# Performance work log

Hardware: AMD Instinct MI355X
Metric: run time of the kernel (lower is better)

The kernel has to match this reference:

```python
import jax, jax.numpy as jnp
import numpy as np

D_MODEL = 1024
N_HEADS = 16
HEAD_DIM = D_MODEL // N_HEADS
LN_EPS = 1e-5


def _linear_init(key, fan_in, fan_out):
    # xavier_uniform for weight, zeros for bias; torch Linear weight is [out, in]
    limit = float(np.sqrt(6.0 / (fan_in + fan_out)))
    w = jax.random.uniform(key, (fan_out, fan_in), jnp.float32, -limit, limit)
    b = jnp.zeros((fan_out,), jnp.float32)
    return w, b


def setup_inputs() -> dict:
    key = jax.random.key(0)
    ks = jax.random.split(key, 8)
    B, S, D = 4, 1024, D_MODEL
    query = jax.random.normal(ks[0], (B, S, D), jnp.float32)
    key_t = jax.random.normal(ks[1], (B, S, D), jnp.float32)
    value = jax.random.normal(ks[2], (B, S, D), jnp.float32)
    Wq, bq = _linear_init(ks[3], D, D)
    Wk, bk = _linear_init(ks[4], D, D)
    Wv, bv = _linear_init(ks[5], D, D)
    Wfq, bfq = _linear_init(ks[6], D, D)
    Wfk, bfk = _linear_init(ks[7], D, D)
    gamma_q = jnp.ones((D,), jnp.float32); beta_q = jnp.zeros((D,), jnp.float32)
    gamma_k = jnp.ones((D,), jnp.float32); beta_k = jnp.zeros((D,), jnp.float32)
    return {"query": query, "key": key_t, "value": value,
            "Wq": Wq, "bq": bq, "Wk": Wk, "bk": bk, "Wv": Wv, "bv": bv,
            "Wfq": Wfq, "bfq": bfq, "Wfk": Wfk, "bfk": bfk,
            "gamma_q": gamma_q, "beta_q": beta_q,
            "gamma_k": gamma_k, "beta_k": beta_k}


def _layernorm(x, gamma, beta):
    mu = jnp.mean(x, axis=-1, keepdims=True)
    var = jnp.mean(jnp.square(x - mu), axis=-1, keepdims=True)
    return (x - mu) * jax.lax.rsqrt(var + LN_EPS) * gamma + beta


def reference(query, key, value, Wq, bq, Wk, bk, Wv, bv, Wfq, bfq, Wfk, bfk,
              gamma_q, beta_q, gamma_k, beta_k):
    B, Sq, D = query.shape
    H, Hd = N_HEADS, HEAD_DIM
    scale = jnp.sqrt(jnp.asarray(Hd, jnp.float32))

    residual_q, residual_k = query, key
    # torch Linear: x @ W.T + b
    q = (query @ Wq.T + bq).reshape(B, Sq, H, Hd).transpose(0, 2, 1, 3)  # [B,H,Sq,Hd]
    k = (key @ Wk.T + bk).reshape(B, -1, H, Hd).transpose(0, 2, 1, 3)    # [B,H,Sk,Hd]
    v = (value @ Wv.T + bv).reshape(B, -1, H, Hd).transpose(0, 2, 1, 3)  # [B,H,Sv,Hd]

    # Q->K attention (dropout disabled / eval mode)
    energy = jnp.einsum('bhqd,bhkd->bhqk', q, k) / scale
    attn_q2k = jax.nn.softmax(energy, axis=-1)
    x_q = jnp.einsum('bhqk,bhkd->bhqd', attn_q2k, v)
    x_q = x_q.transpose(0, 2, 1, 3).reshape(B, Sq, D)

    # K->Q attention (shares V)
    energy_k = jnp.einsum('bhkd,bhqd->bhkq', k, q) / scale
    attn_k2q = jax.nn.softmax(energy_k, axis=-1)
    x_k = jnp.einsum('bhkq,bhqd->bhkd', attn_k2q, v)
    x_k = x_k.transpose(0, 2, 1, 3).reshape(B, -1, D)

    q_out = x_q @ Wfq.T + bfq
    query_out = _layernorm(residual_q + q_out, gamma_q, beta_q)
    k_out = x_k @ Wfk.T + bfk
    key_out = _layernorm(residual_k + k_out, gamma_k, beta_k)
    return (query_out, key_out)
```

## Files before the change

### kernel.cpp

```cpp
#include <hip/hip_runtime.h>

typedef unsigned short u16;
typedef unsigned int u32;
typedef __attribute__((ext_vector_type(8))) short short8;
typedef __attribute__((ext_vector_type(4))) float floatx4;
typedef __attribute__((ext_vector_type(16))) float f32x16;
typedef __attribute__((ext_vector_type(4))) u32 u32x4;

#define AS_GLOBAL __attribute__((address_space(1)))
#define AS_LDS    __attribute__((address_space(3)))

__device__ __forceinline__ float b2f(u16 v) {
  union { u32 u; float f; } x; x.u = ((u32)v) << 16; return x.f;
}
__device__ __forceinline__ u16 f2bf(float f) {
  union { float f; u32 u; } x; x.f = f;
  u32 r = (x.u + 0x7fffu + ((x.u >> 16) & 1u)) >> 16;
  return (u16)r;
}
__device__ __forceinline__ u32 pk2(float lo, float hi) {
  u32 r; asm("v_cvt_pk_bf16_f32 %0, %1, %2" : "=v"(r) : "v"(lo), "v"(hi)); return r;
}
__device__ __forceinline__ float exp2_hw(float x) {
  float r; asm("v_exp_f32 %0, %1" : "=v"(r) : "v"(x)); return r;
}
__device__ __forceinline__ void plswap(u32& a, u32& b) {
  __attribute__((ext_vector_type(2))) unsigned int r =
      __builtin_amdgcn_permlane32_swap(a, b, false, false);
  a = r[0]; b = r[1];
}
__device__ __forceinline__ void gl_lds16(const u16* g, u16* l) {
  __builtin_amdgcn_global_load_lds((const AS_GLOBAL u32*)g, (AS_LDS u32*)l, 16, 0, 0);
}

__global__ __launch_bounds__(256)
void cvt8(const float* __restrict__ s0, const float* __restrict__ s1, const float* __restrict__ s2,
          const float* __restrict__ s3, const float* __restrict__ s4, const float* __restrict__ s5,
          const float* __restrict__ s6, const float* __restrict__ s7,
          u16* __restrict__ d0, u16* __restrict__ d1, u16* __restrict__ d2,
          u16* __restrict__ d3, u16* __restrict__ d4, u16* __restrict__ d5,
          u16* __restrict__ d6, u16* __restrict__ d7, int nbig, int nsmall)
{
  const int z = blockIdx.y;
  const float* s; u16* d; int n;
  switch (z) {
    case 0: s = s0; d = d0; n = nbig; break;
    case 1: s = s1; d = d1; n = nbig; break;
    case 2: s = s2; d = d2; n = nbig; break;
    case 3: s = s3; d = d3; n = nsmall; break;
    case 4: s = s4; d = d4; n = nsmall; break;
    case 5: s = s5; d = d5; n = nsmall; break;
    case 6: s = s6; d = d6; n = nsmall; break;
    default: s = s7; d = d7; n = nsmall; break;
  }
  const size_t idx = ((size_t)blockIdx.x * 256 + threadIdx.x) * 8;
  if (idx >= (size_t)n) return;
  float4 a0 = *(const float4*)(s + idx);
  float4 a1 = *(const float4*)(s + idx + 4);
  u16 t[8];
  t[0] = f2bf(a0.x); t[1] = f2bf(a0.y); t[2] = f2bf(a0.z); t[3] = f2bf(a0.w);
  t[4] = f2bf(a1.x); t[5] = f2bf(a1.y); t[6] = f2bf(a1.z); t[7] = f2bf(a1.w);
  *(uint4*)(d + idx) = *(const uint4*)t;
}

template <int TRANS2>
__global__ __launch_bounds__(256, 3)
void gemm_nt_bias(const u16* __restrict__ A0, const u16* __restrict__ W0, const float* __restrict__ B0, u16* __restrict__ C0,
                  const u16* __restrict__ A1, const u16* __restrict__ W1, const float* __restrict__ B1, u16* __restrict__ C1,
                  const u16* __restrict__ A2, const u16* __restrict__ W2, const float* __restrict__ B2, u16* __restrict__ C2)
{
  constexpr int K = 1024, N = 1024;
  __shared__ __attribute__((aligned(16))) u16 As[128 * 64];
  __shared__ __attribute__((aligned(16))) u16 Bs[128 * 64];

  const int z = blockIdx.z;
  const u16*   A  = z == 0 ? A0 : (z == 1 ? A1 : A2);
  const u16*   W  = z == 0 ? W0 : (z == 1 ? W1 : W2);
  const float* Bi = z == 0 ? B0 : (z == 1 ? B1 : B2);
  u16*         C  = z == 0 ? C0 : (z == 1 ? C1 : C2);

  const int tid  = threadIdx.x;
  const int lane = tid & 63;
  const int wave = tid >> 6;
  const int l32  = lane & 31;
  const int hi   = lane >> 5;
  const int wm = wave >> 1, wn = wave & 1;
  const int m0 = blockIdx.x * 128;
  const int n0 = blockIdx.y * 128;

  f32x16 acc[2][2];
#pragma unroll
  for (int i = 0; i < 2; ++i)
#pragma unroll
    for (int j = 0; j < 2; ++j)
#pragma unroll
      for (int e = 0; e < 16; ++e) acc[i][j][e] = 0.f;

  const int rr = lane >> 3;
  const int s7 = lane & 7;
  int scg[4];
#pragma unroll
  for (int i = 0; i < 4; ++i)
    scg[i] = ((s7 ^ rr ^ ((wave * 32 + i * 8) >> 3)) & 7) << 3;

  const u16* gA = A + (size_t)(m0 + wave * 32 + rr) * K;
  const u16* gW = W + (size_t)(n0 + wave * 32 + rr) * K;

  int offA0[4], offA1[4], offW0[4], offW1[4];
  {
    const int rA0 = wm * 64 + l32,      rA1 = rA0 + 32;
    const int rW0 = wn * 64 + l32,      rW1 = rW0 + 32;
    const int kA0 = (rA0 ^ (rA0 >> 3)) & 7, kA1 = (rA1 ^ (rA1 >> 3)) & 7;
    const int kW0 = (rW0 ^ (rW0 >> 3)) & 7, kW1 = (rW1 ^ (rW1 >> 3)) & 7;
#pragma unroll
    for (int ks = 0; ks < 4; ++ks) {
      const int g = ks * 2 + hi;
      offA0[ks] = rA0 * 64 + ((g ^ kA0) & 7) * 8;
      offA1[ks] = rA1 * 64 + ((g ^ kA1) & 7) * 8;
      offW0[ks] = rW0 * 64 + ((g ^ kW0) & 7) * 8;
      offW1[ks] = rW1 * 64 + ((g ^ kW1) & 7) * 8;
    }
  }

  const bool tr = TRANS2 && (z == 2);

  for (int k0 = 0; k0 < K; k0 += 64) {
#pragma unroll
    for (int i = 0; i < 4; ++i) {
      gl_lds16(gA + (size_t)(i * 8) * K + k0 + scg[i], &As[(wave * 32 + i * 8) * 64]);
      gl_lds16(gW + (size_t)(i * 8) * K + k0 + scg[i], &Bs[(wave * 32 + i * 8) * 64]);
    }
    __syncthreads();
    if (!tr) {
#pragma unroll
      for (int ks = 0; ks < 4; ++ks) {
        short8 fA0 = *(const short8*)&As[offA0[ks]];
        short8 fA1 = *(const short8*)&As[offA1[ks]];
        short8 fW0 = *(const short8*)&Bs[offW0[ks]];
        short8 fW1 = *(const short8*)&Bs[offW1[ks]];
        acc[0][0] = __builtin_amdgcn_mfma_f32_32x32x16_bf16(fW0, fA0, acc[0][0], 0, 0, 0);
        acc[0][1] = __builtin_amdgcn_mfma_f32_32x32x16_bf16(fW1, fA0, acc[0][1], 0, 0, 0);
        acc[1][0] = __builtin_amdgcn_mfma_f32_32x32x16_bf16(fW0, fA1, acc[1][0], 0, 0, 0);
        acc[1][1] = __builtin_amdgcn_mfma_f32_32x32x16_bf16(fW1, fA1, acc[1][1], 0, 0, 0);
      }
    } else {
#pragma unroll
      for (int ks = 0; ks < 4; ++ks) {
        short8 fA0 = *(const short8*)&As[offA0[ks]];
        short8 fA1 = *(const short8*)&As[offA1[ks]];
        short8 fW0 = *(const short8*)&Bs[offW0[ks]];
        short8 fW1 = *(const short8*)&Bs[offW1[ks]];
        acc[0][0] = __builtin_amdgcn_mfma_f32_32x32x16_bf16(fA0, fW0, acc[0][0], 0, 0, 0);
        acc[0][1] = __builtin_amdgcn_mfma_f32_32x32x16_bf16(fA0, fW1, acc[0][1], 0, 0, 0);
        acc[1][0] = __builtin_amdgcn_mfma_f32_32x32x16_bf16(fA1, fW0, acc[1][0], 0, 0, 0);
        acc[1][1] = __builtin_amdgcn_mfma_f32_32x32x16_bf16(fA1, fW1, acc[1][1], 0, 0, 0);
      }
    }
    __syncthreads();
  }

  if (!tr) {
    float4 bb[2][4];
#pragma unroll
    for (int nh = 0; nh < 2; ++nh)
#pragma unroll
      for (int q2 = 0; q2 < 4; ++q2)
        bb[nh][q2] = *(const float4*)&Bi[n0 + wn * 64 + nh * 32 + q2 * 8 + hi * 4];
#pragma unroll
    for (int mh = 0; mh < 2; ++mh) {
      u16* crow = C + (size_t)(m0 + wm * 64 + mh * 32 + l32) * N + n0 + wn * 64;
#pragma unroll
      for (int nh = 0; nh < 2; ++nh)
#pragma unroll
        for (int q2 = 0; q2 < 4; ++q2) {
          uint2 w;
          w.x = pk2(acc[mh][nh][q2 * 4 + 0] + bb[nh][q2].x,
                    acc[mh][nh][q2 * 4 + 1] + bb[nh][q2].y);
          w.y = pk2(acc[mh][nh][q2 * 4 + 2] + bb[nh][q2].z,
                    acc[mh][nh][q2 * 4 + 3] + bb[nh][q2].w);
          *(uint2*)(crow + nh * 32 + q2 * 8 + hi * 4) = w;
        }
    }
  } else {
    const float b0 = Bi[n0 + wn * 64 + l32];
    const float b1 = Bi[n0 + wn * 64 + 32 + l32];
#pragma unroll
    for (int nh = 0; nh < 2; ++nh) {
      const float bbv = nh ? b1 : b0;
      u16* ct = C + (size_t)(n0 + wn * 64 + nh * 32 + l32) * 4096 + m0 + wm * 64;
#pragma unroll
      for (int mh = 0; mh < 2; ++mh)
#pragma unroll
        for (int q2 = 0; q2 < 4; ++q2) {
          uint2 w;
          w.x = pk2(acc[mh][nh][q2 * 4 + 0] + bbv, acc[mh][nh][q2 * 4 + 1] + bbv);
          w.y = pk2(acc[mh][nh][q2 * 4 + 2] + bbv, acc[mh][nh][q2 * 4 + 3] + bbv);
          *(uint2*)(ct + mh * 32 + q2 * 8 + hi * 4) = w;
        }
    }
  }
}

__global__ __launch_bounds__(256, 2)
void flash32(const u16* __restrict__ Qg, const u16* __restrict__ Kg,
             const u16* __restrict__ VTw, u16* __restrict__ OQ, u16* __restrict__ OK)
{
  __shared__ __attribute__((aligned(16))) u16 smem[4 * 4096];

  const int tid = threadIdx.x;
  const int lane = tid & 63;
  const int wave = tid >> 6;
  const int l32 = lane & 31;
  const int hi = lane >> 5;

  const int jlin = blockIdx.x + 4 * (blockIdx.y + 64 * blockIdx.z);
  const int L = (jlin & 7) * 64 + (jlin >> 3);
  const int qx = L & 3;
  const int by = (L >> 2) & 63;
  const int bz = L >> 8;
  const int b = by >> 4, h = by & 15;
  const int q0 = qx * 256;

  const u16* Qw = bz ? Kg : Qg;
  const u16* Kw = bz ? Qg : Kg;
  u16* Ow = bz ? OK : OQ;

  const int rr = lane >> 3;
  const int s7 = lane & 7;

  const u16* Qt = Qw + ((size_t)(b * 1024 + q0)) * 1024 + h * 64;
  const u16* Kt = Kw + ((size_t)(b * 1024)) * 1024 + h * 64;
  const u16* Vt = VTw + ((size_t)(h * 64)) * 4096 + (size_t)b * 1024;

#pragma unroll
  for (int c = 0; c < 8; ++c) {
    const int R = wave * 64 + c * 8;
    const int cg = ((s7 ^ rr ^ (R >> 3)) & 7) << 3;
    gl_lds16(Qt + (size_t)(R + rr) * 1024 + cg, smem + R * 64);
  }
  __syncthreads();

  short8 aqA[4], aqB[4];
  {
    const int qrA = wave * 64 + l32, qrB = qrA + 32;
    const int kA = (qrA ^ (qrA >> 3)) & 7, kB = (qrB ^ (qrB >> 3)) & 7;
    const u16* bA = smem + qrA * 64;
    const u16* bB = smem + qrB * 64;
#pragma unroll
    for (int d2 = 0; d2 < 4; ++d2) {
      const int g = d2 * 2 + hi;
      aqA[d2] = *(const short8*)(bA + ((g ^ kA) & 7) * 8);
      aqB[d2] = *(const short8*)(bB + ((g ^ kB) & 7) * 8);
    }
  }
  __syncthreads();

  const int R0 = wave * 16, R1 = wave * 16 + 8;
  const int cg0 = ((s7 ^ rr ^ (R0 >> 3)) & 7) << 3;
  const int cg1 = ((s7 ^ rr ^ (R1 >> 3)) & 7) << 3;
  {
    u16* kd = smem + wave * 1024;
    u16* vd = smem + 8192 + wave * 1024;
    gl_lds16(Kt + (size_t)(R0 + rr) * 1024 + cg0, kd);
    gl_lds16(Kt + (size_t)(R1 + rr) * 1024 + cg1, kd + 512);
    gl_lds16(Vt + (size_t)(R0 + rr) * 4096 + cg0, vd);
    gl_lds16(Vt + (size_t)(R1 + rr) * 4096 + cg1, vd + 512);
  }
  __syncthreads();

  const int key0 = (l32 ^ (l32 >> 3)) & 7;
  const int key1 = key0 ^ 4;

  int offA[4], offB[4];
#pragma unroll
  for (int j = 0; j < 4; ++j) {
    const int g = j * 2 + hi;
    offA[j] = (l32 * 64 + ((g ^ key0) & 7) * 8) * 2;
    offB[j] = ((32 + l32) * 64 + ((g ^ key1) & 7) * 8) * 2;
  }

  const u16* pK0 = Kt + (size_t)(64 + R0 + rr) * 1024 + cg0;
  const u16* pK1 = Kt + (size_t)(64 + R1 + rr) * 1024 + cg1;
  const u16* pV0 = Vt + (size_t)(R0 + rr) * 4096 + 64 + cg0;
  const u16* pV1 = Vt + (size_t)(R1 + rr) * 4096 + 64 + cg1;

  f32x16 accO0A, accO1A, accO0B, accO1B;
#pragma unroll
  for (int i = 0; i < 16; ++i) {
    accO0A[i] = 0.f; accO1A[i] = 0.f; accO0B[i] = 0.f; accO1B[i] = 0.f;
  }
  f32x16 zeroS;
#pragma unroll
  for (int i = 0; i < 16; ++i) zeroS[i] = 0.f;

  float lsumA = 0.f, lsumB = 0.f;
  const float SCL2 = 0.18033688011112042f;
  const float MFIX2 = 10.098865286222744f;

#define EXP4(SV, o)                                                     \
  SV[o + 0] = exp2_hw(fmaf(SV[o + 0], SCL2, -MFIX2));                   \
  SV[o + 1] = exp2_hw(fmaf(SV[o + 1], SCL2, -MFIX2));                   \
  SV[o + 2] = exp2_hw(fmaf(SV[o + 2], SCL2, -MFIX2));                   \
  SV[o + 3] = exp2_hw(fmaf(SV[o + 3], SCL2, -MFIX2));
#define SUM8(v, o) (((v[o] + v[o + 1]) + (v[o + 2] + v[o + 3])) + \
                    ((v[o + 4] + v[o + 5]) + (v[o + 6] + v[o + 7])))
#define PACK(SV, PFA, PFB)                                              \
  {                                                                     \
    u32 a0 = pk2(SV[0], SV[1]),   a1 = pk2(SV[2], SV[3]);               \
    u32 b0 = pk2(SV[4], SV[5]),   b1 = pk2(SV[6], SV[7]);               \
    u32 c0 = pk2(SV[8], SV[9]),   c1 = pk2(SV[10], SV[11]);             \
    u32 d0 = pk2(SV[12], SV[13]), d1 = pk2(SV[14], SV[15]);             \
    plswap(a0, b0); plswap(a1, b1); plswap(c0, d0); plswap(c1, d1);     \
    u32x4 u0; u0[0] = a0; u0[1] = a1; u0[2] = b0; u0[3] = b1;           \
    u32x4 u1; u1[0] = c0; u1[1] = c1; u1[2] = d0; u1[3] = d1;           \
    PFA = __builtin_bit_cast(short8, u0);                               \
    PFB = __builtin_bit_cast(short8, u1);                               \
  }

  for (int jt = 0; jt < 16; ++jt) {
    const int cur = jt & 1;
    const char* ksb = (const char*)smem + cur * 8192;
    const char* vtb = (const char*)smem + 16384 + cur * 8192;

    if (jt < 15) {
      u16* kd = smem + (cur ^ 1) * 4096 + wave * 1024;
      u16* vd = smem + 8192 + (cur ^ 1) * 4096 + wave * 1024;
      gl_lds16(pK0, kd);
      gl_lds16(pK1, kd + 512);
      gl_lds16(pV0, vd);
      gl_lds16(pV1, vd + 512);
      pK0 += 65536; pK1 += 65536; pV0 += 64; pV1 += 64;
    }

    f32x16 sA0, sB0, sA1, sB1;
    {
      short8 kf = *(const short8*)(ksb + offA[0]);
      sA0 = __builtin_amdgcn_mfma_f32_32x32x16_bf16(kf, aqA[0], zeroS, 0, 0, 0);
      sB0 = __builtin_amdgcn_mfma_f32_32x32x16_bf16(kf, aqB[0], zeroS, 0, 0, 0);
    }
#pragma unroll
    for (int d2 = 1; d2 < 4; ++d2) {
      short8 kf = *(const short8*)(ksb + offA[d2]);
      sA0 = __builtin_amdgcn_mfma_f32_32x32x16_bf16(kf, aqA[d2], sA0, 0, 0, 0);
      sB0 = __builtin_amdgcn_mfma_f32_32x32x16_bf16(kf, aqB[d2], sB0, 0, 0, 0);
    }

    short8 va0 = *(const short8*)(vtb + offA[0]);
    short8 vb0 = *(const short8*)(vtb + offB[0]);
    short8 va1 = *(const short8*)(vtb + offA[1]);
    short8 vb1 = *(const short8*)(vtb + offB[1]);

    {
      short8 kf = *(const short8*)(ksb + offB[0]);
      sA1 = __builtin_amdgcn_mfma_f32_32x32x16_bf16(kf, aqA[0], zeroS, 0, 0, 0);
      EXP4(sA0, 0)
      sB1 = __builtin_amdgcn_mfma_f32_32x32x16_bf16(kf, aqB[0], zeroS, 0, 0, 0);
      EXP4(sB0, 0)
    }
#pragma unroll
    for (int d2 = 1; d2 < 4; ++d2) {
      short8 kf = *(const short8*)(ksb + offB[d2]);
      sA1 = __builtin_amdgcn_mfma_f32_32x32x16_bf16(kf, aqA[d2], sA1, 0, 0, 0);
      EXP4(sA0, d2 * 4)
      sB1 = __builtin_amdgcn_mfma_f32_32x32x16_bf16(kf, aqB[d2], sB1, 0, 0, 0);
      EXP4(sB0, d2 * 4)
    }

    {
      short8 pfaA, pfbA, pfaB, pfbB;
      PACK(sA0, pfaA, pfbA)
      EXP4(sA1, 0) EXP4(sA1, 4)
      PACK(sB0, pfaB, pfbB)
      EXP4(sA1, 8) EXP4(sA1, 12)
      accO0A = __builtin_amdgcn_mfma_f32_32x32x16_bf16(va0, pfaA, accO0A, 0, 0, 0);
      accO1A = __builtin_amdgcn_mfma_f32_32x32x16_bf16(vb0, pfaA, accO1A, 0, 0, 0);
      lsumA += SUM8(sA0, 0) + SUM8(sA0, 8);
      EXP4(sB1, 0) EXP4(sB1, 4)
      accO0B = __builtin_amdgcn_mfma_f32_32x32x16_bf16(va0, pfaB, accO0B, 0, 0, 0);
      accO1B = __builtin_amdgcn_mfma_f32_32x32x16_bf16(vb0, pfaB, accO1B, 0, 0, 0);
      lsumB += SUM8(sB0, 0) + SUM8(sB0, 8);
      EXP4(sB1, 8) EXP4(sB1, 12)
      short8 va2 = *(const short8*)(vtb + offA[2]);
      short8 vb2 = *(const short8*)(vtb + offB[2]);
      short8 va3 = *(const short8*)(vtb + offA[3]);
      short8 vb3 = *(const short8*)(vtb + offB[3]);
      accO0A = __builtin_amdgcn_mfma_f32_32x32x16_bf16(va1, pfbA, accO0A, 0, 0, 0);
      accO1A = __builtin_amdgcn_mfma_f32_32x32x16_bf16(vb1, pfbA, accO1A, 0, 0, 0);
      accO0B = __builtin_amdgcn_mfma_f32_32x32x16_bf16(va1, pfbB, accO0B, 0, 0, 0);
      accO1B = __builtin_amdgcn_mfma_f32_32x32x16_bf16(vb1, pfbB, accO1B, 0, 0, 0);

      short8 qfaA, qfbA, qfaB, qfbB;
      PACK(sA1, qfaA, qfbA)
      PACK(sB1, qfaB, qfbB)
      accO0A = __builtin_amdgcn_mfma_f32_32x32x16_bf16(va2, qfaA, accO0A, 0, 0, 0);
      accO1A = __builtin_amdgcn_mfma_f32_32x32x16_bf16(vb2, qfaA, accO1A, 0, 0, 0);
      lsumA += SUM8(sA1, 0) + SUM8(sA1, 8);
      accO0B = __builtin_amdgcn_mfma_f32_32x32x16_bf16(va2, qfaB, accO0B, 0, 0, 0);
      accO1B = __builtin_amdgcn_mfma_f32_32x32x16_bf16(vb2, qfaB, accO1B, 0, 0, 0);
      lsumB += SUM8(sB1, 0) + SUM8(sB1, 8);
      accO0A = __builtin_amdgcn_mfma_f32_32x32x16_bf16(va3, qfbA, accO0A, 0, 0, 0);
      accO1A = __builtin_amdgcn_mfma_f32_32x32x16_bf16(vb3, qfbA, accO1A, 0, 0, 0);
      accO0B = __builtin_amdgcn_mfma_f32_32x32x16_bf16(va3, qfbB, accO0B, 0, 0, 0);
      accO1B = __builtin_amdgcn_mfma_f32_32x32x16_bf16(vb3, qfbB, accO1B, 0, 0, 0);
    }
    __syncthreads();
  }
#undef EXP4
#undef SUM8
#undef PACK

  const float invlA = 1.f / (lsumA + __shfl_xor(lsumA, 32, 64));
  const float invlB = 1.f / (lsumB + __shfl_xor(lsumB, 32, 64));

  u16* orowA = Ow + ((size_t)(b * 1024 + q0 + wave * 64 + l32)) * 1024 + h * 64 + hi * 4;
  u16* orowB = orowA + (size_t)32 * 1024;
#pragma unroll
  for (int rg = 0; rg < 4; ++rg) {
    uint2 w0;
    w0.x = pk2(accO0A[rg * 4 + 0] * invlA, accO0A[rg * 4 + 1] * invlA);
    w0.y = pk2(accO0A[rg * 4 + 2] * invlA, accO0A[rg * 4 + 3] * invlA);
    *(uint2*)(orowA + rg * 8) = w0;
    uint2 w1;
    w1.x = pk2(accO1A[rg * 4 + 0] * invlA, accO1A[rg * 4 + 1] * invlA);
    w1.y = pk2(accO1A[rg * 4 + 2] * invlA, accO1A[rg * 4 + 3] * invlA);
    *(uint2*)(orowA + 32 + rg * 8) = w1;
    uint2 w2;
    w2.x = pk2(accO0B[rg * 4 + 0] * invlB, accO0B[rg * 4 + 1] * invlB);
    w2.y = pk2(accO0B[rg * 4 + 2] * invlB, accO0B[rg * 4 + 3] * invlB);
    *(uint2*)(orowB + rg * 8) = w2;
    uint2 w3;
    w3.x = pk2(accO1B[rg * 4 + 0] * invlB, accO1B[rg * 4 + 1] * invlB);
    w3.y = pk2(accO1B[rg * 4 + 2] * invlB, accO1B[rg * 4 + 3] * invlB);
    *(uint2*)(orowB + 32 + rg * 8) = w3;
  }
}

__global__ __launch_bounds__(256)
void ln_residual(const u16* __restrict__ TQ, const u16* __restrict__ TK,
                 const float* __restrict__ Rq, const float* __restrict__ Rk,
                 const float* __restrict__ gq, const float* __restrict__ bq,
                 const float* __restrict__ gk, const float* __restrict__ bk,
                 float* __restrict__ out)
{
  const int row = blockIdx.x;
  const u16 *X; const float *R, *G, *Bt; float* O;
  if (row < 4096) {
    X = TQ + (size_t)row * 1024; R = Rq + (size_t)row * 1024;
    G = gq; Bt = bq; O = out + (size_t)row * 1024;
  } else {
    const int r2 = row - 4096;
    X = TK + (size_t)r2 * 1024; R = Rk + (size_t)r2 * 1024;
    G = gk; Bt = bk; O = out + (size_t)4096 * 1024 + (size_t)r2 * 1024;
  }
  const int c0 = threadIdx.x * 4;
  const uint2 xv = *(const uint2*)(X + c0);
  const float4 rv = *(const float4*)(R + c0);
  float v[4];
  v[0] = b2f((u16)(xv.x & 0xffff)) + rv.x;
  v[1] = b2f((u16)(xv.x >> 16)) + rv.y;
  v[2] = b2f((u16)(xv.y & 0xffff)) + rv.z;
  v[3] = b2f((u16)(xv.y >> 16)) + rv.w;
  float sum = (v[0] + v[1]) + (v[2] + v[3]);
  float sumsq = (v[0] * v[0] + v[1] * v[1]) + (v[2] * v[2] + v[3] * v[3]);
#pragma unroll
  for (int sh = 1; sh < 64; sh <<= 1) {
    sum += __shfl_xor(sum, sh, 64);
    sumsq += __shfl_xor(sumsq, sh, 64);
  }
  __shared__ float sm[8];
  const int wave = threadIdx.x >> 6, lane = threadIdx.x & 63;
  if (lane == 0) { sm[wave] = sum; sm[4 + wave] = sumsq; }
  __syncthreads();
  sum = (sm[0] + sm[1]) + (sm[2] + sm[3]);
  sumsq = (sm[4] + sm[5]) + (sm[6] + sm[7]);
  const float mu = sum * (1.f / 1024.f);
  const float var = sumsq * (1.f / 1024.f) - mu * mu;
  const float rstd = rsqrtf(var + 1e-5f);
  const float4 gv = *(const float4*)(G + c0);
  const float4 bv = *(const float4*)(Bt + c0);
  float4 ov;
  ov.x = (v[0] - mu) * rstd * gv.x + bv.x;
  ov.y = (v[1] - mu) * rstd * gv.y + bv.y;
  ov.z = (v[2] - mu) * rstd * gv.z + bv.z;
  ov.w = (v[3] - mu) * rstd * gv.w + bv.w;
  *(float4*)(O + c0) = ov;
}

extern "C" void kernel_launch(void* const* d_in, const int* in_sizes, int n_in,
                              void* d_out, int out_size, void* d_ws, size_t ws_size,
                              hipStream_t stream)
{
  const float* query = (const float*)d_in[0];
  const float* key   = (const float*)d_in[1];
  const float* value = (const float*)d_in[2];
  const float* Wq  = (const float*)d_in[3];  const float* bq  = (const float*)d_in[4];
  const float* Wk  = (const float*)d_in[5];  const float* bk  = (const float*)d_in[6];
  const float* Wv  = (const float*)d_in[7];  const float* bv  = (const float*)d_in[8];
  const float* Wfq = (const float*)d_in[9];  const float* bfq = (const float*)d_in[10];
  const float* Wfk = (const float*)d_in[11]; const float* bfk = (const float*)d_in[12];
  const float* gq = (const float*)d_in[13];  const float* betaq = (const float*)d_in[14];
  const float* gk = (const float*)d_in[15];  const float* betak = (const float*)d_in[16];
  float* out = (float*)d_out;
  u16* ws  = (u16*)d_ws;

  const size_t SZ = (size_t)4096 * 1024;
  const size_t WZ = (size_t)1024 * 1024;
  u16* Qb  = ws;
  u16* Kb  = ws + SZ;
  u16* VT  = ws + 2 * SZ;
  u16* Wqb = ws + 3 * SZ;
  u16* Wkb = Wqb + WZ;
  u16* Wvb = Wkb + WZ;
  u16* Wfqb = Wvb + WZ;
  u16* Wfkb = Wfqb + WZ;
  u16* qbf = (u16*)out;
  u16* kbf = qbf + SZ;
  u16* vbf = kbf + SZ;
  u16* XQ = (u16*)out;
  u16* XK = (u16*)out + SZ;
  u16* TQ = Qb;
  u16* TK = Kb;

  cvt8<<<dim3(2048, 8), 256, 0, stream>>>(query, key, value, Wq, Wk, Wv, Wfq, Wfk,
                                          qbf, kbf, vbf, Wqb, Wkb, Wvb, Wfqb, Wfkb,
                                          (int)SZ, (int)WZ);
  gemm_nt_bias<1><<<dim3(32, 8, 3), 256, 0, stream>>>(qbf, Wqb, bq, Qb,
                                                      kbf, Wkb, bk, Kb,
                                                      vbf, Wvb, bv, VT);
  flash32<<<dim3(4, 64, 2), 256, 0, stream>>>(Qb, Kb, VT, XQ, XK);
  gemm_nt_bias<0><<<dim3(32, 8, 2), 256, 0, stream>>>(XQ, Wfqb, bfq, TQ,
                                                      XK, Wfkb, bfk, TK,
                                                      XK, Wfkb, bfk, TK);
  ln_residual<<<dim3(8192), 256, 0, stream>>>(TQ, TK, query, key,
                                              gq, betaq, gk, betak, out);
}
```

Baseline: 257.8 us.

## Double-buffer LDS tiles in projection GEMM to overlap loads with MFMA

The bias GEMM now keeps two LDS buffers for the A and W tiles. It prefetches the next K-slice into the alternate buffer while MFMAs consume the current one, which removes one barrier per iteration and hides global-to-LDS latency. Shared memory per block doubles, so the launch bound drops from 3 to 2 blocks per CU. That costs occupancy and could offset the overlap gain.

After: 259.3 us. Within noise of the previous version (+0.6%).

```diff
diff --git a/kernel.cpp b/kernel.cpp
--- a/kernel.cpp
+++ b/kernel.cpp
@@ -64,14 +64,14 @@
 }
 
 template <int TRANS2>
-__global__ __launch_bounds__(256, 3)
+__global__ __launch_bounds__(256, 2)
 void gemm_nt_bias(const u16* __restrict__ A0, const u16* __restrict__ W0, const float* __restrict__ B0, u16* __restrict__ C0,
                   const u16* __restrict__ A1, const u16* __restrict__ W1, const float* __restrict__ B1, u16* __restrict__ C1,
                   const u16* __restrict__ A2, const u16* __restrict__ W2, const float* __restrict__ B2, u16* __restrict__ C2)
 {
   constexpr int K = 1024, N = 1024;
-  __shared__ __attribute__((aligned(16))) u16 As[128 * 64];
-  __shared__ __attribute__((aligned(16))) u16 Bs[128 * 64];
+  __shared__ __attribute__((aligned(16))) u16 As[2][128 * 64];
+  __shared__ __attribute__((aligned(16))) u16 Bs[2][128 * 64];
 
   const int z = blockIdx.z;
   const u16*   A  = z == 0 ? A0 : (z == 1 ? A1 : A2);
@@ -124,20 +124,32 @@
 
   const bool tr = TRANS2 && (z == 2);
 
-  for (int k0 = 0; k0 < K; k0 += 64) {
-#pragma unroll
-    for (int i = 0; i < 4; ++i) {
-      gl_lds16(gA + (size_t)(i * 8) * K + k0 + scg[i], &As[(wave * 32 + i * 8) * 64]);
-      gl_lds16(gW + (size_t)(i * 8) * K + k0 + scg[i], &Bs[(wave * 32 + i * 8) * 64]);
-    }
-    __syncthreads();
+#pragma unroll
+  for (int i = 0; i < 4; ++i) {
+    gl_lds16(gA + (size_t)(i * 8) * K + scg[i], &As[0][(wave * 32 + i * 8) * 64]);
+    gl_lds16(gW + (size_t)(i * 8) * K + scg[i], &Bs[0][(wave * 32 + i * 8) * 64]);
+  }
+  __syncthreads();
+
+  for (int t = 0; t < 16; ++t) {
+    const int cur = t & 1;
+    if (t < 15) {
+      const int k1 = (t + 1) * 64;
+#pragma unroll
+      for (int i = 0; i < 4; ++i) {
+        gl_lds16(gA + (size_t)(i * 8) * K + k1 + scg[i], &As[cur ^ 1][(wave * 32 + i * 8) * 64]);
+        gl_lds16(gW + (size_t)(i * 8) * K + k1 + scg[i], &Bs[cur ^ 1][(wave * 32 + i * 8) * 64]);
+      }
+    }
+    const u16* as = As[cur];
+    const u16* bs = Bs[cur];
     if (!tr) {
 #pragma unroll
       for (int ks = 0; ks < 4; ++ks) {
-        short8 fA0 = *(const short8*)&As[offA0[ks]];
-        short8 fA1 = *(const short8*)&As[offA1[ks]];
-        short8 fW0 = *(const short8*)&Bs[offW0[ks]];
-        short8 fW1 = *(const short8*)&Bs[offW1[ks]];
+        short8 fA0 = *(const short8*)&as[offA0[ks]];
+        short8 fA1 = *(const short8*)&as[offA1[ks]];
+        short8 fW0 = *(const short8*)&bs[offW0[ks]];
+        short8 fW1 = *(const short8*)&bs[offW1[ks]];
         acc[0][0] = __builtin_amdgcn_mfma_f32_32x32x16_bf16(fW0, fA0, acc[0][0], 0, 0, 0);
         acc[0][1] = __builtin_amdgcn_mfma_f32_32x32x16_bf16(fW1, fA0, acc[0][1], 0, 0, 0);
         acc[1][0] = __builtin_amdgcn_mfma_f32_32x32x16_bf16(fW0, fA1, acc[1][0], 0, 0, 0);
@@ -146,10 +158,10 @@
     } else {
 #pragma unroll
       for (int ks = 0; ks < 4; ++ks) {
-        short8 fA0 = *(const short8*)&As[offA0[ks]];
-        short8 fA1 = *(const short8*)&As[offA1[ks]];
-        short8 fW0 = *(const short8*)&Bs[offW0[ks]];
-        short8 fW1 = *(const short8*)&Bs[offW1[ks]];
+        short8 fA0 = *(const short8*)&as[offA0[ks]];
+        short8 fA1 = *(const short8*)&as[offA1[ks]];
+        short8 fW0 = *(const short8*)&bs[offW0[ks]];
+        short8 fW1 = *(const short8*)&bs[offW1[ks]];
         acc[0][0] = __builtin_amdgcn_mfma_f32_32x32x16_bf16(fA0, fW0, acc[0][0], 0, 0, 0);
         acc[0][1] = __builtin_amdgcn_mfma_f32_32x32x16_bf16(fA0, fW1, acc[0][1], 0, 0, 0);
         acc[1][0] = __builtin_amdgcn_mfma_f32_32x32x16_bf16(fA1, fW0, acc[1][0], 0, 0, 0);
```
